# Kernel optimization log

Hardware: AMD Instinct MI355X
Metric: run time of the kernel (lower is better)

The kernel has to match this reference:

```python
import jax, jax.numpy as jnp
import numpy as np

# ---- Instant-NGP 4D hash-grid constants (hard-coded in the torch module) ----
L = 16; F = 2; LOG2_T = 19; T = 1 << LOG2_T; N_MIN = 8; N_MAX = 2048
B_SCALE = np.exp(np.log(N_MAX / N_MIN) / (L - 1))
AABB = 1.0
PRIMES = np.array([1, 2654435761, 805459861, 3674351687], dtype=np.uint32)  # tcnn fast_hash primes (4D)
CORNERS = np.array([[(c >> d) & 1 for d in range(4)] for c in range(16)], dtype=np.int32)  # [16,4]


def _level_res(l):
    scale = np.exp2(l * np.log2(B_SCALE)) * N_MIN - 1.0  # tcnn grid_scale
    res = int(np.ceil(scale)) + 1
    return float(scale), res


def hash_encode(x, grid):
    """x: [N,4] in [0,1]; grid: [L,T,F]. Returns [N, L*F]."""
    feats = []
    for l in range(L):
        scale, res = _level_res(l)
        pos = x * scale + 0.5                      # tcnn position mapping
        g = jnp.floor(pos)
        frac = pos - g                             # [N,4]
        gi = g.astype(jnp.int32)
        corner = gi[:, None, :] + CORNERS[None]    # [N,16,4]
        w = jnp.prod(jnp.where(CORNERS[None].astype(bool), frac[:, None, :], 1.0 - frac[:, None, :]), axis=-1)  # [N,16]
        if res ** 4 <= T:
            # dense (stride) indexing for coarse levels, as tcnn does
            stride = jnp.array([1, res, res * res, res ** 3], dtype=jnp.int32)
            idx = jnp.minimum(jnp.sum(corner * stride, axis=-1), T - 1)
        else:
            cu = corner.astype(jnp.uint32)
            h = (cu[..., 0] * PRIMES[0]) ^ (cu[..., 1] * PRIMES[1]) ^ (cu[..., 2] * PRIMES[2]) ^ (cu[..., 3] * PRIMES[3])
            idx = (h & jnp.uint32(T - 1)).astype(jnp.int32)
        vals = grid[l][idx]                        # [N,16,F] irregular gather
        feats.append(jnp.sum(w[..., None] * vals, axis=1))  # quadrilinear interp -> [N,F]
    return jnp.concatenate(feats, axis=-1)         # [N,32]


def sh_deg4(d):
    """tcnn SphericalHarmonics degree 4; d in [-1,1]^3. Returns [N,16]."""
    x, y, z = d[:, 0], d[:, 1], d[:, 2]
    xy, xz, yz = x * y, x * z, y * z
    x2, y2, z2 = x * x, y * y, z * z
    return jnp.stack([
        jnp.full_like(x, 0.28209479177387814),
        -0.48860251190291987 * y,
        0.48860251190291987 * z,
        -0.48860251190291987 * x,
        1.0925484305920792 * xy,
        -1.0925484305920792 * yz,
        0.94617469575755997 * z2 - 0.31539156525251999,
        -1.0925484305920792 * xz,
        0.54627421529603959 * x2 - 0.54627421529603959 * y2,
        0.59004358992664352 * y * (-3.0 * x2 + y2),
        2.8906114426405538 * xy * z,
        0.45704579946446572 * y * (1.0 - 5.0 * z2),
        0.3731763325901154 * z * (5.0 * z2 - 3.0),
        0.45704579946446572 * x * (1.0 - 5.0 * z2),
        1.4453057213202769 * z * (x2 - y2),
        0.59004358992664352 * x * (-x2 + 3.0 * y2),
    ], axis=-1)


def setup_inputs() -> dict:
    key = jax.random.key(0)
    ks = jax.random.split(key, 8)
    N = 262144
    original_xyzs = jax.random.uniform(ks[0], (N, 4), dtype=jnp.float32)
    dirs = jax.random.uniform(ks[1], (N, 3), dtype=jnp.float32)
    # tcnn hash-grid init: uniform [-1e-4, 1e-4]
    grid = jax.random.uniform(ks[2], (L, T, F), dtype=jnp.float32, minval=-1e-4, maxval=1e-4)
    def he(k, o, i):
        return jax.random.normal(k, (o, i), dtype=jnp.float32) * np.sqrt(2.0 / i).astype(np.float32)
    W1 = he(ks[3], 64, 32)
    W2 = he(ks[4], 16, 64)
    Wc1 = he(ks[5], 64, 32)
    Wc2 = he(ks[6], 64, 64)
    Wc3 = he(ks[7], 3, 64)
    return {"original_xyzs": original_xyzs, "dirs": dirs, "grid": grid,
            "W1": W1, "W2": W2, "Wc1": Wc1, "Wc2": Wc2, "Wc3": Wc3}


def reference(original_xyzs, dirs, grid, W1, W2, Wc1, Wc2, Wc3):
    ts = original_xyzs[:, 3:4]
    xyz = (original_xyzs[:, :3] + AABB) / AABB / 2.0   # -> [0,1]
    inp = jnp.concatenate([xyz, ts], axis=1)           # [N,4]
    hr = hash_encode(inp, grid)                        # [N,32]
    # xyz_encoder: CutlassMLP 32->64 (ReLU) ->16, no biases
    h = jax.nn.relu(hr @ W1.T) @ W2.T                  # [N,16]
    sigma = jnp.exp(h[:, 0])                           # TruncExp forward
    sh = sh_deg4(dirs * 2.0 - 1.0)                     # [N,16]
    ci = jnp.concatenate([sh, h], axis=1)              # [N,32]
    color = jax.nn.sigmoid(jax.nn.relu(jax.nn.relu(ci @ Wc1.T) @ Wc2.T) @ Wc3.T)  # [N,3]
    return color, sigma
```

## Files before the change

kernel.cpp:

```cpp
#include <hip/hip_runtime.h>
#include <math.h>

#define THREADS 256

static __device__ __constant__ float kScale[16] = {
    7.0f,          10.57815398f,  15.75670563f,  23.25146503f,
    34.09839735f,  49.79683366f,  72.51669472f,  105.39843246f,
    152.98718950f, 221.86092960f, 321.53978800f, 465.80191600f,
    674.58804640f, 976.75780270f, 1414.07882380f, 2047.0f};
static __device__ __constant__ int kRes[4] = {8, 12, 17, 25};

__global__ void __launch_bounds__(THREADS)
htrf_fused(const float* __restrict__ xyzs, const float* __restrict__ dirs,
           const float* __restrict__ grid, const float* __restrict__ W1,
           const float* __restrict__ W2, const float* __restrict__ Wc1,
           const float* __restrict__ Wc2, const float* __restrict__ Wc3,
           float* __restrict__ out, int N) {
  __shared__ float sbuf[THREADS * 33];
  const int tid = threadIdx.x;
  const int n = blockIdx.x * THREADS + tid;
  if (n >= N) return;
  float* __restrict__ my = sbuf + tid * 33;

  const float4 p = reinterpret_cast<const float4*>(xyzs)[n];
  const float q0 = (p.x + 1.0f) * 0.5f;
  const float q1 = (p.y + 1.0f) * 0.5f;
  const float q2 = (p.z + 1.0f) * 0.5f;
  const float q3 = p.w;

  #pragma unroll 1
  for (int l = 0; l < 16; ++l) {
    const float s = kScale[l];
    const float pos0 = fmaf(q0, s, 0.5f);
    const float pos1 = fmaf(q1, s, 0.5f);
    const float pos2 = fmaf(q2, s, 0.5f);
    const float pos3 = fmaf(q3, s, 0.5f);
    const float fl0 = floorf(pos0), fl1 = floorf(pos1);
    const float fl2 = floorf(pos2), fl3 = floorf(pos3);
    const float f0 = pos0 - fl0, f1 = pos1 - fl1;
    const float f2 = pos2 - fl2, f3 = pos3 - fl3;
    const int g0 = (int)fl0, g1 = (int)fl1, g2 = (int)fl2, g3 = (int)fl3;

    float wxy[4], wzt[4];
    {
      const float u0 = 1.0f - f0, u1 = 1.0f - f1, u2 = 1.0f - f2, u3 = 1.0f - f3;
      wxy[0] = u0 * u1; wxy[1] = f0 * u1; wxy[2] = u0 * f1; wxy[3] = f0 * f1;
      wzt[0] = u2 * u3; wzt[1] = f2 * u3; wzt[2] = u2 * f3; wzt[3] = f2 * f3;
    }

    unsigned idx[16];
    if (l < 4) {
      const int r = kRes[l];
      const int r2 = r * r, r3 = r2 * r;
      const int x0 = g0, x1 = g0 + 1;
      const int y0 = g1 * r, y1 = (g1 + 1) * r;
      const int z0 = g2 * r2, z1 = (g2 + 1) * r2;
      const int t0 = g3 * r3, t1 = (g3 + 1) * r3;
      const int sxy[4] = {x0 + y0, x1 + y0, x0 + y1, x1 + y1};
      const int szt[4] = {z0 + t0, z1 + t0, z0 + t1, z1 + t1};
      #pragma unroll
      for (int cc = 0; cc < 16; ++cc) {
        const int v = sxy[cc & 3] + szt[cc >> 2];
        idx[cc] = (unsigned)(v < (1 << 19) - 1 ? v : (1 << 19) - 1);
      }
    } else {
      const unsigned x0 = (unsigned)g0,               x1 = (unsigned)(g0 + 1);
      const unsigned y0 = (unsigned)g1 * 2654435761u, y1 = (unsigned)(g1 + 1) * 2654435761u;
      const unsigned z0 = (unsigned)g2 * 805459861u,  z1 = (unsigned)(g2 + 1) * 805459861u;
      const unsigned t0 = (unsigned)g3 * 3674351687u, t1 = (unsigned)(g3 + 1) * 3674351687u;
      const unsigned sxy[4] = {x0 ^ y0, x1 ^ y0, x0 ^ y1, x1 ^ y1};
      const unsigned szt[4] = {z0 ^ t0, z1 ^ t0, z0 ^ t1, z1 ^ t1};
      #pragma unroll
      for (int cc = 0; cc < 16; ++cc)
        idx[cc] = (sxy[cc & 3] ^ szt[cc >> 2]) & ((1u << 19) - 1u);
    }

    const float2* __restrict__ gl =
        reinterpret_cast<const float2*>(grid) + ((size_t)l << 19);
    float2 vv[16];
    #pragma unroll
    for (int cc = 0; cc < 16; ++cc) vv[cc] = gl[idx[cc]];
    float a0 = 0.0f, a1 = 0.0f;
    #pragma unroll
    for (int cc = 0; cc < 16; ++cc) {
      const float w = wxy[cc & 3] * wzt[cc >> 2];
      a0 = fmaf(w, vv[cc].x, a0);
      a1 = fmaf(w, vv[cc].y, a1);
    }
    my[2 * l]     = a0;
    my[2 * l + 1] = a1;
  }

  float fr[32];
  #pragma unroll
  for (int k = 0; k < 32; ++k) fr[k] = my[k];

  float h[16];
  #pragma unroll
  for (int i = 0; i < 16; ++i) h[i] = 0.0f;

  #pragma unroll 1
  for (int j = 0; j < 64; ++j) {
    const float* __restrict__ w = W1 + j * 32;
    float b0 = 0.f, b1 = 0.f, b2 = 0.f, b3 = 0.f;
    #pragma unroll
    for (int k = 0; k < 32; k += 4) {
      b0 = fmaf(fr[k + 0], w[k + 0], b0);
      b1 = fmaf(fr[k + 1], w[k + 1], b1);
      b2 = fmaf(fr[k + 2], w[k + 2], b2);
      b3 = fmaf(fr[k + 3], w[k + 3], b3);
    }
    const float act = fmaxf((b0 + b1) + (b2 + b3), 0.0f);
    #pragma unroll
    for (int i = 0; i < 16; ++i) h[i] = fmaf(act, W2[i * 64 + j], h[i]);
  }
  const float sigma = expf(h[0]);

  const float dxr = dirs[3 * n + 0], dyr = dirs[3 * n + 1], dzr = dirs[3 * n + 2];
  const float x = fmaf(dxr, 2.0f, -1.0f);
  const float y = fmaf(dyr, 2.0f, -1.0f);
  const float z = fmaf(dzr, 2.0f, -1.0f);
  const float xy = x * y, xz = x * z, yz = y * z;
  const float x2 = x * x, y2 = y * y, z2 = z * z;
  float ci[32];
  ci[0]  = 0.28209479177387814f;
  ci[1]  = -0.48860251190291987f * y;
  ci[2]  = 0.48860251190291987f * z;
  ci[3]  = -0.48860251190291987f * x;
  ci[4]  = 1.0925484305920792f * xy;
  ci[5]  = -1.0925484305920792f * yz;
  ci[6]  = 0.94617469575756f * z2 - 0.31539156525252f;
  ci[7]  = -1.0925484305920792f * xz;
  ci[8]  = 0.5462742152960396f * x2 - 0.5462742152960396f * y2;
  ci[9]  = 0.5900435899266435f * y * (-3.0f * x2 + y2);
  ci[10] = 2.890611442640554f * xy * z;
  ci[11] = 0.4570457994644657f * y * (1.0f - 5.0f * z2);
  ci[12] = 0.3731763325901154f * z * (5.0f * z2 - 3.0f);
  ci[13] = 0.4570457994644657f * x * (1.0f - 5.0f * z2);
  ci[14] = 1.445305721320277f * z * (x2 - y2);
  ci[15] = 0.5900435899266435f * x * (-x2 + 3.0f * y2);
  #pragma unroll
  for (int i = 0; i < 16; ++i) ci[16 + i] = h[i];

  float c2p[64];
  #pragma unroll
  for (int i = 0; i < 64; ++i) c2p[i] = 0.0f;

  #pragma unroll 1
  for (int j = 0; j < 64; ++j) {
    const float* __restrict__ w = Wc1 + j * 32;
    float b0 = 0.f, b1 = 0.f, b2 = 0.f, b3 = 0.f;
    #pragma unroll
    for (int k = 0; k < 32; k += 4) {
      b0 = fmaf(ci[k + 0], w[k + 0], b0);
      b1 = fmaf(ci[k + 1], w[k + 1], b1);
      b2 = fmaf(ci[k + 2], w[k + 2], b2);
      b3 = fmaf(ci[k + 3], w[k + 3], b3);
    }
    const float act = fmaxf((b0 + b1) + (b2 + b3), 0.0f);
    #pragma unroll
    for (int i = 0; i < 64; ++i) c2p[i] = fmaf(act, Wc2[i * 64 + j], c2p[i]);
  }

  float l0a = 0.f, l0b = 0.f, l1a = 0.f, l1b = 0.f, l2a = 0.f, l2b = 0.f;
  #pragma unroll
  for (int i = 0; i < 64; i += 2) {
    const float a0r = fmaxf(c2p[i], 0.0f);
    const float a1r = fmaxf(c2p[i + 1], 0.0f);
    l0a = fmaf(a0r, Wc3[0 * 64 + i], l0a);
    l0b = fmaf(a1r, Wc3[0 * 64 + i + 1], l0b);
    l1a = fmaf(a0r, Wc3[1 * 64 + i], l1a);
    l1b = fmaf(a1r, Wc3[1 * 64 + i + 1], l1b);
    l2a = fmaf(a0r, Wc3[2 * 64 + i], l2a);
    l2b = fmaf(a1r, Wc3[2 * 64 + i + 1], l2b);
  }
  const float col0 = 1.0f / (1.0f + expf(-(l0a + l0b)));
  const float col1 = 1.0f / (1.0f + expf(-(l1a + l1b)));
  const float col2 = 1.0f / (1.0f + expf(-(l2a + l2b)));

  out[3 * n + 0] = col0;
  out[3 * n + 1] = col1;
  out[3 * n + 2] = col2;
  out[3 * N + n] = sigma;
}

extern "C" void kernel_launch(void* const* d_in, const int* in_sizes, int n_in,
                              void* d_out, int out_size, void* d_ws, size_t ws_size,
                              hipStream_t stream) {
  const int N = in_sizes[0] / 4;
  htrf_fused<<<dim3((N + THREADS - 1) / THREADS), dim3(THREADS), 0, stream>>>(
      (const float*)d_in[0], (const float*)d_in[1], (const float*)d_in[2],
      (const float*)d_in[3], (const float*)d_in[4], (const float*)d_in[5],
      (const float*)d_in[6], (const float*)d_in[7], (float*)d_out, N);
}
```

Baseline: 377.5 us.

## Split hashed-level encoding into a level-parallel kernel before the MLP

Adds a separate encode kernel that handles the 12 hashed levels with one level per block. Block IDs are interleaved so that concurrent blocks work on different levels and nearby chunks, which aims to keep each level's 4 MB table slice resident in cache and to expose more parallel gathers. Features are written to the workspace as float2 per level. The MLP kernel computes the four dense levels inline, reads the hashed features back, and runs the MLPs. This adds a workspace round trip and a second launch, and falls back to the old fused kernel when the workspace is too small.

```diff
diff --git a/kernel.cpp b/kernel.cpp
--- a/kernel.cpp
+++ b/kernel.cpp
@@ -2,6 +2,7 @@
 #include <math.h>
 
 #define THREADS 256
+#define TMASK ((1u << 19) - 1u)
 
 static __device__ __constant__ float kScale[16] = {
     7.0f,          10.57815398f,  15.75670563f,  23.25146503f,
@@ -10,17 +11,24 @@
     674.58804640f, 976.75780270f, 1414.07882380f, 2047.0f};
 static __device__ __constant__ int kRes[4] = {8, 12, 17, 25};
 
-__global__ void __launch_bounds__(THREADS)
-htrf_fused(const float* __restrict__ xyzs, const float* __restrict__ dirs,
-           const float* __restrict__ grid, const float* __restrict__ W1,
-           const float* __restrict__ W2, const float* __restrict__ Wc1,
-           const float* __restrict__ Wc2, const float* __restrict__ Wc3,
-           float* __restrict__ out, int N) {
-  __shared__ float sbuf[THREADS * 33];
-  const int tid = threadIdx.x;
-  const int n = blockIdx.x * THREADS + tid;
+__global__ void __launch_bounds__(THREADS, 6)
+htrf_encode(const float* __restrict__ xyzs, const float* __restrict__ grid,
+            float2* __restrict__ feat, int N, int CH, int H0) {
+  const int b = blockIdx.x;
+  const int x = b & 7;
+  const int r = b >> 3;
+  int level, chunk;
+  if (r < CH) {
+    level = 4 + x;
+    chunk = r;
+  } else {
+    const int j = r - CH;
+    level = 12 + (x >> 1);
+    chunk = (x & 1) ? (H0 + j) : j;
+    if (chunk >= CH) return;
+  }
+  const int n = chunk * THREADS + threadIdx.x;
   if (n >= N) return;
-  float* __restrict__ my = sbuf + tid * 33;
 
   const float4 p = reinterpret_cast<const float4*>(xyzs)[n];
   const float q0 = (p.x + 1.0f) * 0.5f;
@@ -28,8 +36,67 @@
   const float q2 = (p.z + 1.0f) * 0.5f;
   const float q3 = p.w;
 
-  #pragma unroll 1
-  for (int l = 0; l < 16; ++l) {
+  const float s = kScale[level];
+  const float pos0 = fmaf(q0, s, 0.5f);
+  const float pos1 = fmaf(q1, s, 0.5f);
+  const float pos2 = fmaf(q2, s, 0.5f);
+  const float pos3 = fmaf(q3, s, 0.5f);
+  const float fl0 = floorf(pos0), fl1 = floorf(pos1);
+  const float fl2 = floorf(pos2), fl3 = floorf(pos3);
+  const float f0 = pos0 - fl0, f1 = pos1 - fl1;
+  const float f2 = pos2 - fl2, f3 = pos3 - fl3;
+  const int g0 = (int)fl0, g1 = (int)fl1, g2 = (int)fl2, g3 = (int)fl3;
+
+  float wxy[4], wzt[4];
+  {
+    const float u0 = 1.0f - f0, u1 = 1.0f - f1, u2 = 1.0f - f2, u3 = 1.0f - f3;
+    wxy[0] = u0 * u1; wxy[1] = f0 * u1; wxy[2] = u0 * f1; wxy[3] = f0 * f1;
+    wzt[0] = u2 * u3; wzt[1] = f2 * u3; wzt[2] = u2 * f3; wzt[3] = f2 * f3;
+  }
+
+  const unsigned hx0 = (unsigned)g0,               hx1 = (unsigned)(g0 + 1);
+  const unsigned hy0 = (unsigned)g1 * 2654435761u, hy1 = (unsigned)(g1 + 1) * 2654435761u;
+  const unsigned hz0 = (unsigned)g2 * 805459861u,  hz1 = (unsigned)(g2 + 1) * 805459861u;
+  const unsigned ht0 = (unsigned)g3 * 3674351687u, ht1 = (unsigned)(g3 + 1) * 3674351687u;
+  const unsigned sxy[4] = {hx0 ^ hy0, hx1 ^ hy0, hx0 ^ hy1, hx1 ^ hy1};
+  const unsigned szt[4] = {hz0 ^ ht0, hz1 ^ ht0, hz0 ^ ht1, hz1 ^ ht1};
+
+  const float2* __restrict__ gl =
+      reinterpret_cast<const float2*>(grid) + ((size_t)level << 19);
+  float2 vv[16];
+  #pragma unroll
+  for (int cc = 0; cc < 16; ++cc) {
+    const unsigned idx = (sxy[cc & 3] ^ szt[cc >> 2]) & TMASK;
+    vv[cc] = gl[idx];
+  }
+  float a0 = 0.0f, a1 = 0.0f;
+  #pragma unroll
+  for (int cc = 0; cc < 16; ++cc) {
+    const float w = wxy[cc & 3] * wzt[cc >> 2];
+    a0 = fmaf(w, vv[cc].x, a0);
+    a1 = fmaf(w, vv[cc].y, a1);
+  }
+  feat[(size_t)(level - 4) * N + n] = make_float2(a0, a1);
+}
+
+__global__ void __launch_bounds__(THREADS)
+htrf_mlp(const float* __restrict__ xyzs, const float* __restrict__ dirs,
+         const float* __restrict__ grid, const float* __restrict__ W1,
+         const float* __restrict__ W2, const float* __restrict__ Wc1,
+         const float* __restrict__ Wc2, const float* __restrict__ Wc3,
+         const float2* __restrict__ feat, float* __restrict__ out, int N) {
+  const int n = blockIdx.x * THREADS + threadIdx.x;
+  if (n >= N) return;
+
+  const float4 p = reinterpret_cast<const float4*>(xyzs)[n];
+  const float q0 = (p.x + 1.0f) * 0.5f;
+  const float q1 = (p.y + 1.0f) * 0.5f;
+  const float q2 = (p.z + 1.0f) * 0.5f;
+  const float q3 = p.w;
+
+  float fr[32];
+  #pragma unroll
+  for (int l = 0; l < 4; ++l) {
     const float s = kScale[l];
     const float pos0 = fmaf(q0, s, 0.5f);
     const float pos1 = fmaf(q1, s, 0.5f);
@@ -47,39 +114,23 @@
       wxy[0] = u0 * u1; wxy[1] = f0 * u1; wxy[2] = u0 * f1; wxy[3] = f0 * f1;
       wzt[0] = u2 * u3; wzt[1] = f2 * u3; wzt[2] = u2 * f3; wzt[3] = f2 * f3;
     }
-
-    unsigned idx[16];
-    if (l < 4) {
-      const int r = kRes[l];
-      const int r2 = r * r, r3 = r2 * r;
-      const int x0 = g0, x1 = g0 + 1;
-      const int y0 = g1 * r, y1 = (g1 + 1) * r;
-      const int z0 = g2 * r2, z1 = (g2 + 1) * r2;
-      const int t0 = g3 * r3, t1 = (g3 + 1) * r3;
-      const int sxy[4] = {x0 + y0, x1 + y0, x0 + y1, x1 + y1};
-      const int szt[4] = {z0 + t0, z1 + t0, z0 + t1, z1 + t1};
-      #pragma unroll
-      for (int cc = 0; cc < 16; ++cc) {
-        const int v = sxy[cc & 3] + szt[cc >> 2];
-        idx[cc] = (unsigned)(v < (1 << 19) - 1 ? v : (1 << 19) - 1);
-      }
-    } else {
-      const unsigned x0 = (unsigned)g0,               x1 = (unsigned)(g0 + 1);
-      const unsigned y0 = (unsigned)g1 * 2654435761u, y1 = (unsigned)(g1 + 1) * 2654435761u;
-      const unsigned z0 = (unsigned)g2 * 805459861u,  z1 = (unsigned)(g2 + 1) * 805459861u;
-      const unsigned t0 = (unsigned)g3 * 3674351687u, t1 = (unsigned)(g3 + 1) * 3674351687u;
-      const unsigned sxy[4] = {x0 ^ y0, x1 ^ y0, x0 ^ y1, x1 ^ y1};
-      const unsigned szt[4] = {z0 ^ t0, z1 ^ t0, z0 ^ t1, z1 ^ t1};
-      #pragma unroll
-      for (int cc = 0; cc < 16; ++cc)
-        idx[cc] = (sxy[cc & 3] ^ szt[cc >> 2]) & ((1u << 19) - 1u);
-    }
-
+    const int rr = kRes[l];
+    const int r2 = rr * rr, r3 = r2 * rr;
+    const int ix0 = g0, ix1 = g0 + 1;
+    const int iy0 = g1 * rr, iy1 = (g1 + 1) * rr;
+    const int iz0 = g2 * r2, iz1 = (g2 + 1) * r2;
+    const int it0 = g3 * r3, it1 = (g3 + 1) * r3;
+    const int sxy[4] = {ix0 + iy0, ix1 + iy0, ix0 + iy1, ix1 + iy1};
+    const int szt[4] = {iz0 + it0, iz1 + it0, iz0 + it1, iz1 + it1};
     const float2* __restrict__ gl =
         reinterpret_cast<const float2*>(grid) + ((size_t)l << 19);
     float2 vv[16];
     #pragma unroll
-    for (int cc = 0; cc < 16; ++cc) vv[cc] = gl[idx[cc]];
+    for (int cc = 0; cc < 16; ++cc) {
+      const int v = sxy[cc & 3] + szt[cc >> 2];
+      const int idx = v < (int)TMASK ? v : (int)TMASK;
+      vv[cc] = gl[idx];
+    }
     float a0 = 0.0f, a1 = 0.0f;
     #pragma unroll
     for (int cc = 0; cc < 16; ++cc) {
@@ -87,13 +138,15 @@
       a0 = fmaf(w, vv[cc].x, a0);
       a1 = fmaf(w, vv[cc].y, a1);
     }
-    my[2 * l]     = a0;
-    my[2 * l + 1] = a1;
-  }
-
-  float fr[32];
-  #pragma unroll
-  for (int k = 0; k < 32; ++k) fr[k] = my[k];
+    fr[2 * l] = a0;
+    fr[2 * l + 1] = a1;
+  }
+  #pragma unroll
+  for (int l = 0; l < 12; ++l) {
+    const float2 v = feat[(size_t)l * N + n];
+    fr[8 + 2 * l] = v.x;
+    fr[9 + 2 * l] = v.y;
+  }
 
   float h[16];
   #pragma unroll
@@ -184,12 +237,200 @@
   out[3 * N + n] = sigma;
 }
 
+__global__ void __launch_bounds__(THREADS)
+htrf_fused(const float* __restrict__ xyzs, const float* __restrict__ dirs,
+           const float* __restrict__ grid, const float* __restrict__ W1,
+           const float* __restrict__ W2, const float* __restrict__ Wc1,
+           const float* __restrict__ Wc2, const float* __restrict__ Wc3,
+           float* __restrict__ out, int N) {
+  __shared__ float sbuf[THREADS * 33];
+  const int tid = threadIdx.x;
+  const int n = blockIdx.x * THREADS + tid;
+  if (n >= N) return;
+  float* __restrict__ my = sbuf + tid * 33;
+
+  const float4 p = reinterpret_cast<const float4*>(xyzs)[n];
+  const float q0 = (p.x + 1.0f) * 0.5f;
+  const float q1 = (p.y + 1.0f) * 0.5f;
+  const float q2 = (p.z + 1.0f) * 0.5f;
+  const float q3 = p.w;
+
+  #pragma unroll 1
+  for (int l = 0; l < 16; ++l) {
+    const float s = kScale[l];
+    const float pos0 = fmaf(q0, s, 0.5f);
+    const float pos1 = fmaf(q1, s, 0.5f);
+    const float pos2 = fmaf(q2, s, 0.5f);
+    const float pos3 = fmaf(q3, s, 0.5f);
+    const float fl0 = floorf(pos0), fl1 = floorf(pos1);
+    const float fl2 = floorf(pos2), fl3 = floorf(pos3);
+    const float f0 = pos0 - fl0, f1 = pos1 - fl1;
+    const float f2 = pos2 - fl2, f3 = pos3 - fl3;
+    const int g0 = (int)fl0, g1 = (int)fl1, g2 = (int)fl2, g3 = (int)fl3;
+
+    float wxy[4], wzt[4];
+    {
+      const float u0 = 1.0f - f0, u1 = 1.0f - f1, u2 = 1.0f - f2, u3 = 1.0f - f3;
+      wxy[0] = u0 * u1; wxy[1] = f0 * u1; wxy[2] = u0 * f1; wxy[3] = f0 * f1;
+      wzt[0] = u2 * u3; wzt[1] = f2 * u3; wzt[2] = u2 * f3; wzt[3] = f2 * f3;
+    }
+
+    unsigned idx[16];
+    if (l < 4) {
+      const int rr = kRes[l];
+      const int r2 = rr * rr, r3 = r2 * rr;
+      const int ix0 = g0, ix1 = g0 + 1;
+      const int iy0 = g1 * rr, iy1 = (g1 + 1) * rr;
+      const int iz0 = g2 * r2, iz1 = (g2 + 1) * r2;
+      const int it0 = g3 * r3, it1 = (g3 + 1) * r3;
+      const int sxy[4] = {ix0 + iy0, ix1 + iy0, ix0 + iy1, ix1 + iy1};
+      const int szt[4] = {iz0 + it0, iz1 + it0, iz0 + it1, iz1 + it1};
+      #pragma unroll
+      for (int cc = 0; cc < 16; ++cc) {
+        const int v = sxy[cc & 3] + szt[cc >> 2];
+        idx[cc] = (unsigned)(v < (int)TMASK ? v : (int)TMASK);
+      }
+    } else {
+      const unsigned hx0 = (unsigned)g0,               hx1 = (unsigned)(g0 + 1);
+      const unsigned hy0 = (unsigned)g1 * 2654435761u, hy1 = (unsigned)(g1 + 1) * 2654435761u;
+      const unsigned hz0 = (unsigned)g2 * 805459861u,  hz1 = (unsigned)(g2 + 1) * 805459861u;
+      const unsigned ht0 = (unsigned)g3 * 3674351687u, ht1 = (unsigned)(g3 + 1) * 3674351687u;
+      const unsigned sxy[4] = {hx0 ^ hy0, hx1 ^ hy0, hx0 ^ hy1, hx1 ^ hy1};
+      const unsigned szt[4] = {hz0 ^ ht0, hz1 ^ ht0, hz0 ^ ht1, hz1 ^ ht1};
+      #pragma unroll
+      for (int cc = 0; cc < 16; ++cc)
+        idx[cc] = (sxy[cc & 3] ^ szt[cc >> 2]) & TMASK;
+    }
+
+    const float2* __restrict__ gl =
+        reinterpret_cast<const float2*>(grid) + ((size_t)l << 19);
+    float2 vv[16];
+    #pragma unroll
+    for (int cc = 0; cc < 16; ++cc) vv[cc] = gl[idx[cc]];
+    float a0 = 0.0f, a1 = 0.0f;
+    #pragma unroll
+    for (int cc = 0; cc < 16; ++cc) {
+      const float w = wxy[cc & 3] * wzt[cc >> 2];
+      a0 = fmaf(w, vv[cc].x, a0);
+      a1 = fmaf(w, vv[cc].y, a1);
+    }
+    my[2 * l] = a0;
+    my[2 * l + 1] = a1;
+  }
+
+  float fr[32];
+  #pragma unroll
+  for (int k = 0; k < 32; ++k) fr[k] = my[k];
+
+  float h[16];
+  #pragma unroll
+  for (int i = 0; i < 16; ++i) h[i] = 0.0f;
+
+  #pragma unroll 1
+  for (int j = 0; j < 64; ++j) {
+    const float* __restrict__ w = W1 + j * 32;
+    float b0 = 0.f, b1 = 0.f, b2 = 0.f, b3 = 0.f;
+    #pragma unroll
+    for (int k = 0; k < 32; k += 4) {
+      b0 = fmaf(fr[k + 0], w[k + 0], b0);
+      b1 = fmaf(fr[k + 1], w[k + 1], b1);
+      b2 = fmaf(fr[k + 2], w[k + 2], b2);
+      b3 = fmaf(fr[k + 3], w[k + 3], b3);
+    }
+    const float act = fmaxf((b0 + b1) + (b2 + b3), 0.0f);
+    #pragma unroll
+    for (int i = 0; i < 16; ++i) h[i] = fmaf(act, W2[i * 64 + j], h[i]);
+  }
+  const float sigma = expf(h[0]);
+
+  const float dxr = dirs[3 * n + 0], dyr = dirs[3 * n + 1], dzr = dirs[3 * n + 2];
+  const float x = fmaf(dxr, 2.0f, -1.0f);
+  const float y = fmaf(dyr, 2.0f, -1.0f);
+  const float z = fmaf(dzr, 2.0f, -1.0f);
+  const float xy = x * y, xz = x * z, yz = y * z;
+  const float x2 = x * x, y2 = y * y, z2 = z * z;
+  float ci[32];
+  ci[0]  = 0.28209479177387814f;
+  ci[1]  = -0.48860251190291987f * y;
+  ci[2]  = 0.48860251190291987f * z;
+  ci[3]  = -0.48860251190291987f * x;
+  ci[4]  = 1.0925484305920792f * xy;
+  ci[5]  = -1.0925484305920792f * yz;
+  ci[6]  = 0.94617469575756f * z2 - 0.31539156525252f;
+  ci[7]  = -1.0925484305920792f * xz;
+  ci[8]  = 0.5462742152960396f * x2 - 0.5462742152960396f * y2;
+  ci[9]  = 0.5900435899266435f * y * (-3.0f * x2 + y2);
+  ci[10] = 2.890611442640554f * xy * z;
+  ci[11] = 0.4570457994644657f * y * (1.0f - 5.0f * z2);
+  ci[12] = 0.3731763325901154f * z * (5.0f * z2 - 3.0f);
+  ci[13] = 0.4570457994644657f * x * (1.0f - 5.0f * z2);
+  ci[14] = 1.445305721320277f * z * (x2 - y2);
+  ci[15] = 0.5900435899266435f * x * (-x2 + 3.0f * y2);
+  #pragma unroll
+  for (int i = 0; i < 16; ++i) ci[16 + i] = h[i];
+
+  float c2p[64];
+  #pragma unroll
+  for (int i = 0; i < 64; ++i) c2p[i] = 0.0f;
+
+  #pragma unroll 1
+  for (int j = 0; j < 64; ++j) {
+    const float* __restrict__ w = Wc1 + j * 32;
+    float b0 = 0.f, b1 = 0.f, b2 = 0.f, b3 = 0.f;
+    #pragma unroll
+    for (int k = 0; k < 32; k += 4) {
+      b0 = fmaf(ci[k + 0], w[k + 0], b0);
+      b1 = fmaf(ci[k + 1], w[k + 1], b1);
+      b2 = fmaf(ci[k + 2], w[k + 2], b2);
+      b3 = fmaf(ci[k + 3], w[k + 3], b3);
+    }
+    const float act = fmaxf((b0 + b1) + (b2 + b3), 0.0f);
+    #pragma unroll
+    for (int i = 0; i < 64; ++i) c2p[i] = fmaf(act, Wc2[i * 64 + j], c2p[i]);
+  }
+
+  float l0a = 0.f, l0b = 0.f, l1a = 0.f, l1b = 0.f, l2a = 0.f, l2b = 0.f;
+  #pragma unroll
+  for (int i = 0; i < 64; i += 2) {
+    const float a0r = fmaxf(c2p[i], 0.0f);
+    const float a1r = fmaxf(c2p[i + 1], 0.0f);
+    l0a = fmaf(a0r, Wc3[0 * 64 + i], l0a);
+    l0b = fmaf(a1r, Wc3[0 * 64 + i + 1], l0b);
+    l1a = fmaf(a0r, Wc3[1 * 64 + i], l1a);
+    l1b = fmaf(a1r, Wc3[1 * 64 + i + 1], l1b);
+    l2a = fmaf(a0r, Wc3[2 * 64 + i], l2a);
+    l2b = fmaf(a1r, Wc3[2 * 64 + i + 1], l2b);
+  }
+  const float col0 = 1.0f / (1.0f + expf(-(l0a + l0b)));
+  const float col1 = 1.0f / (1.0f + expf(-(l1a + l1b)));
+  const float col2 = 1.0f / (1.0f + expf(-(l2a + l2b)));
+
+  out[3 * n + 0] = col0;
+  out[3 * n + 1] = col1;
+  out[3 * n + 2] = col2;
+  out[3 * N + n] = sigma;
+}
+
 extern "C" void kernel_launch(void* const* d_in, const int* in_sizes, int n_in,
                               void* d_out, int out_size, void* d_ws, size_t ws_size,
                               hipStream_t stream) {
   const int N = in_sizes[0] / 4;
-  htrf_fused<<<dim3((N + THREADS - 1) / THREADS), dim3(THREADS), 0, stream>>>(
-      (const float*)d_in[0], (const float*)d_in[1], (const float*)d_in[2],
-      (const float*)d_in[3], (const float*)d_in[4], (const float*)d_in[5],
-      (const float*)d_in[6], (const float*)d_in[7], (float*)d_out, N);
+  const size_t need = (size_t)12 * (size_t)N * sizeof(float2);
+  if (ws_size >= need) {
+    const int CH = (N + THREADS - 1) / THREADS;
+    const int H0 = (CH + 1) / 2;
+    const int NB = 8 * (CH + H0);
+    htrf_encode<<<dim3(NB), dim3(THREADS), 0, stream>>>(
+        (const float*)d_in[0], (const float*)d_in[2], (float2*)d_ws, N, CH, H0);
+    htrf_mlp<<<dim3((N + THREADS - 1) / THREADS), dim3(THREADS), 0, stream>>>(
+        (const float*)d_in[0], (const float*)d_in[1], (const float*)d_in[2],
+        (const float*)d_in[3], (const float*)d_in[4], (const float*)d_in[5],
+        (const float*)d_in[6], (const float*)d_in[7], (const float2*)d_ws,
+        (float*)d_out, N);
+  } else {
+    htrf_fused<<<dim3((N + THREADS - 1) / THREADS), dim3(THREADS), 0, stream>>>(
+        (const float*)d_in[0], (const float*)d_in[1], (const float*)d_in[2],
+        (const float*)d_in[3], (const float*)d_in[4], (const float*)d_in[5],
+        (const float*)d_in[6], (const float*)d_in[7], (float*)d_out, N);
+  }
 }
```

Result: slower. 393.5 us (+4.3%).
